# Kernel optimization log

Hardware: AMD Instinct MI355X
Metric: run time of the kernel (lower is better)

Reference implementation:

```python
import jax, jax.numpy as jnp
import numpy as np

B, H, P, D, NF = 4, 8, 196, 64, 8


def setup_inputs() -> dict:
    key = jax.random.key(0)
    ks = jax.random.split(key, 10)
    grid = (jnp.arange(NF * 5, dtype=jnp.float32) + 1.0).reshape(5, NF)
    inv = 1.0 / np.sqrt(D)
    return {
        "q": jax.random.normal(ks[0], (B, H, P, D), jnp.float32),
        "k": jax.random.normal(ks[1], (B, H, P, D), jnp.float32),
        "scale": jnp.ones((1,), jnp.float32),  # accepted but unused (as in original)
        "grid": grid,
        "grid_outer": grid,
        "base_weight": jax.random.uniform(ks[2], (D, D), jnp.float32),
        "coef_q": jax.random.uniform(ks[3], (D, NF, 5), jnp.float32),
        "coef_k": jax.random.uniform(ks[4], (D, NF, 5), jnp.float32),
        "coef_qk": jax.random.uniform(ks[5], (P * P, NF, 5), jnp.float32),
        "scale_base": jnp.ones((1, H, 5, P, D), jnp.float32),
        "scale_sp": jnp.ones((1, H, 5, P, D), jnp.float32),
        "coef_qk_outer": jnp.ones((1, 1, 5, P, P), jnp.float32),
        "lin_q_w": jax.random.uniform(ks[6], (5 * D, D), jnp.float32, -inv, inv),
        "lin_q_b": jax.random.uniform(ks[7], (5 * D,), jnp.float32, -inv, inv),
        "lin_k_w": jax.random.uniform(ks[8], (5 * D, D), jnp.float32, -inv, inv),
        "lin_k_b": jax.random.uniform(ks[9], (5 * D,), jnp.float32, -inv, inv),
    }


def reference(q, k, scale, grid, grid_outer, base_weight, coef_q, coef_k, coef_qk,
              scale_base, scale_sp, coef_qk_outer, lin_q_w, lin_q_b, lin_k_w, lin_k_b):
    b, h, p, d = q.shape
    nf = grid.shape[1]
    qf = q.reshape(-1, d)
    kf = k.reshape(-1, d)
    # lin_q / lin_k -> [B*H*P, 5, D]
    q5 = (qf @ lin_q_w.T + lin_q_b).reshape(-1, 5, d)
    k5 = (kf @ lin_k_w.T + lin_k_b).reshape(-1, 5, d)
    # base path (note: reshape [BHP,5,D] -> [B,H,5,P,D] is a raw row-major remap, as in torch)
    base_q = (jax.nn.silu(q5) @ base_weight.T).reshape(b, h, 5, p, d)
    base_k = (jax.nn.silu(k5) @ base_weight.T).reshape(b, h, 5, p, d)
    # inner sin-basis expansion: sin(grid * x) weighted by coef, summed over num_f
    cq = jnp.transpose(coef_q, (2, 1, 0))  # [5, nf, d]
    ck = jnp.transpose(coef_k, (2, 1, 0))
    sin_q = jnp.sin(grid[None, :, :, None] * q5[:, :, None, :])  # [BHP,5,nf,d]
    f_q = (sin_q * cq[None]).reshape(b, h, 5, nf, p, d).sum(3)   # [B,H,5,P,D]
    sin_k = jnp.sin(grid[None, :, :, None] * k5[:, :, None, :])
    f_k = (sin_k * ck[None]).reshape(b, h, 5, nf, p, d).sum(3)
    f_q = f_q * scale_sp + base_q * scale_base
    f_k = f_k * scale_sp + base_k * scale_base
    # sum_d(sigmoid(q)_d + sigmoid(k)_d) == sum_d sig(q) + sum_d sig(k): outer add of reductions
    aq = jax.nn.sigmoid(f_q).sum(-1)  # [B,H,5,P]
    ak = jax.nn.sigmoid(f_k).sum(-1)
    qk = (aq[..., :, None] + ak[..., None, :]).reshape(b * h, 5, p * p)
    # outer sin-basis expansion over the P*P score map
    cqk = jnp.transpose(coef_qk, (2, 1, 0))  # [5, nf, P*P]
    sin_qk = jnp.sin(grid_outer[None, :, :, None] * qk[:, :, None, :])  # [BH,5,nf,PP]
    f = (sin_qk * cqk[None]).reshape(b, h, 5, nf, p, p).sum(3)  # [B,H,5,P,P]
    f = (f * coef_qk_outer).sum(2)  # [B,H,P,P]
    return jax.nn.softmax(f, axis=-1)
```

## Files before the change

kernel.cpp:

```cpp
#include <hip/hip_runtime.h>
#include <math.h>

#define BHP 6272

__global__ __launch_bounds__(256) void k0w_pack(
    const float* __restrict__ Wq, const float* __restrict__ Wk,
    const float* __restrict__ BW, float4* __restrict__ Wq4,
    float4* __restrict__ Wk4, float4* __restrict__ BW4)
{
  const int e = blockIdx.x * 256 + threadIdx.x;
  if (e < 5120) {
    const int o = e % 320, c4 = e / 320;
    Wq4[e] = *reinterpret_cast<const float4*>(Wq + o * 64 + c4 * 4);
  } else if (e < 10240) {
    const int e2 = e - 5120;
    const int o = e2 % 320, c4 = e2 / 320;
    Wk4[e2] = *reinterpret_cast<const float4*>(Wk + o * 64 + c4 * 4);
  } else if (e < 11264) {
    const int e2 = e - 10240;
    const int d = e2 % 64, c4 = e2 / 64;
    BW4[e2] = *reinterpret_cast<const float4*>(BW + d * 64 + c4 * 4);
  }
}

__global__ __launch_bounds__(320) void k1_lin_base(
    const float* __restrict__ qx, const float* __restrict__ kx,
    const float4* __restrict__ Wq4, const float* __restrict__ bq_,
    const float4* __restrict__ Wk4, const float* __restrict__ bk_,
    const float4* __restrict__ BW4,
    float* __restrict__ y5q, float* __restrict__ y5k,
    float* __restrict__ baseq, float* __restrict__ basek)
{
  const bool kside = blockIdx.x >= (BHP / 8);
  const float* x = kside ? kx : qx;
  const float4* W4 = kside ? Wk4 : Wq4;
  const float* bias = kside ? bk_ : bq_;
  float* y5 = kside ? y5k : y5q;
  float* basef = kside ? basek : baseq;
  const int r0 = (kside ? blockIdx.x - BHP / 8 : blockIdx.x) * 8;

  __shared__ float xs[8][64];
  __shared__ float sy[8][320];
  const int t = threadIdx.x;
  for (int idx = t; idx < 8 * 64; idx += 320)
    xs[idx >> 6][idx & 63] = x[(size_t)(r0 + (idx >> 6)) * 64 + (idx & 63)];
  __syncthreads();

  const int o = t;
  float4 w[16];
  {
#pragma unroll
    for (int c4 = 0; c4 < 16; ++c4) w[c4] = W4[c4 * 320 + o];
    float acc[8];
#pragma unroll
    for (int rr = 0; rr < 8; ++rr) acc[rr] = 0.f;
#pragma unroll
    for (int c4 = 0; c4 < 16; ++c4) {
#pragma unroll
      for (int rr = 0; rr < 8; ++rr) {
        const float4 x4 = *reinterpret_cast<const float4*>(&xs[rr][c4 * 4]);
        acc[rr] = fmaf(x4.x, w[c4].x, acc[rr]);
        acc[rr] = fmaf(x4.y, w[c4].y, acc[rr]);
        acc[rr] = fmaf(x4.z, w[c4].z, acc[rr]);
        acc[rr] = fmaf(x4.w, w[c4].w, acc[rr]);
      }
    }
    const float bb = bias[o];
#pragma unroll
    for (int rr = 0; rr < 8; ++rr) {
      const float y = acc[rr] + bb;
      y5[(size_t)(r0 + rr) * 320 + o] = y;
      sy[rr][o] = y / (1.f + __expf(-y));
    }
  }
  __syncthreads();
  {
    const int s = o >> 6, d = o & 63;
#pragma unroll
    for (int c4 = 0; c4 < 16; ++c4) w[c4] = BW4[c4 * 64 + d];
    float acc[8];
#pragma unroll
    for (int rr = 0; rr < 8; ++rr) acc[rr] = 0.f;
#pragma unroll
    for (int c4 = 0; c4 < 16; ++c4) {
#pragma unroll
      for (int rr = 0; rr < 8; ++rr) {
        const float4 x4 =
            *reinterpret_cast<const float4*>(&sy[rr][s * 64 + c4 * 4]);
        acc[rr] = fmaf(x4.x, w[c4].x, acc[rr]);
        acc[rr] = fmaf(x4.y, w[c4].y, acc[rr]);
        acc[rr] = fmaf(x4.z, w[c4].z, acc[rr]);
        acc[rr] = fmaf(x4.w, w[c4].w, acc[rr]);
      }
    }
#pragma unroll
    for (int rr = 0; rr < 8; ++rr)
      basef[(size_t)(r0 + rr) * 320 + o] = acc[rr];
  }
}

__global__ __launch_bounds__(1024) void k2_act(
    const float* __restrict__ y5q, const float* __restrict__ bq,
    const float* __restrict__ y5k, const float* __restrict__ bk,
    const float* __restrict__ gridI,
    const float* __restrict__ cq, const float* __restrict__ ck,
    const float* __restrict__ ssp, const float* __restrict__ sbase,
    float* __restrict__ aq, float* __restrict__ ak)
{
  __shared__ float cl[40][65];
  __shared__ float gli[40];
  const int t = threadIdx.x;
  const int wave = t >> 6, lane = t & 63;
  const int gi = blockIdx.x * 16 + wave;
  const bool kside = gi >= 31360;
  const int idx = kside ? gi - 31360 : gi;

  {
    const float* coef = kside ? ck : cq;
    for (int e = t; e < 2560; e += 1024) {
      const int d = e / 40, r = e % 40;
      const int f = r / 5, s = r % 5;
      cl[s * 8 + f][d] = coef[e];
    }
    if (t < 40) gli[t] = gridI[t];
  }
  __syncthreads();

  const int p2 = idx % 196;
  const int s2 = (idx / 196) % 5;
  const int bh = idx / 980;
  const int h = bh & 7;
  const int d = lane;
  const int i0 = s2 * 196 + p2;
  const float* y5 = kside ? y5k : y5q;
  const float* basef = kside ? bk : bq;
  const float basev =
      basef[(size_t)(bh * 196 + i0 / 5) * 320 + (i0 % 5) * 64 + d];

  const int j0 = s2 * 1568 + p2;
  int p = j0 / 40;
  int m = j0 % 40;
  const float* y5b = y5 + (size_t)bh * 196 * 320 + d;
  float fv = 0.f;
#pragma unroll
  for (int f2 = 0; f2 < 8; ++f2) {
    const float g = gli[m];
    const float qv = y5b[p * 320 + (m >> 3) * 64];
    fv = fmaf(__sinf(g * qv), cl[m][d], fv);
    p += 4; m += 36;
    if (m >= 40) { m -= 40; p += 1; }
  }
  const int so = ((h * 5 + s2) * 196 + p2) * 64 + d;
  const float v = fv * ssp[so] + basev * sbase[so];
  float sg = 1.f / (1.f + __expf(-v));
#pragma unroll
  for (int off = 32; off > 0; off >>= 1) sg += __shfl_xor(sg, off);
  if (lane == 0) (kside ? ak : aq)[idx] = sg;
}

__global__ __launch_bounds__(256) void k2b_tab(
    const float* __restrict__ aq, const float* __restrict__ ak,
    const float* __restrict__ go, float2* __restrict__ tq,
    float2* __restrict__ tk)
{
  const int n = blockIdx.x * 256 + threadIdx.x;
  const bool kside = n >= 250880;
  const int i2 = kside ? n - 250880 : n;
  const int p = i2 % 196;
  const int m = (i2 / 196) % 40;
  const int bh = i2 / 7840;
  const float g = rintf(go[m]);
  const float a = (kside ? ak : aq)[bh * 980 + (m >> 3) * 196 + p];
  const float n0 = rintf(a * 0.15915494309f);
  float r = fmaf(n0, -6.28318548f, a);
  r = fmaf(n0, 1.74845553e-7f, r);
  const float u = g * r;
  float2* tab = kside ? tk : tq;
  tab[bh * 7840 + m * 196 + p] = make_float2(__sinf(u), __cosf(u));
}

__global__ __launch_bounds__(256) void k0_fuse(
    const float* __restrict__ cqk, const float* __restrict__ cqo,
    float* __restrict__ F)
{
  const int i = blockIdx.x;
  const int t = threadIdx.x;
  __shared__ float ld[196 * 41];
  const float4* src = reinterpret_cast<const float4*>(cqk + (size_t)i * 7840);
  for (int e4 = t; e4 < 1960; e4 += 256) {
    const float4 v = src[e4];
    const int flat = e4 * 4;
    const int j = flat / 40, m0 = flat % 40;
    float* dst = &ld[j * 41 + m0];
    dst[0] = v.x; dst[1] = v.y; dst[2] = v.z; dst[3] = v.w;
  }
  __syncthreads();
  for (int e = t; e < 7840; e += 256) {
    const int mq = e / 196, j = e % 196;
    const int s = mq >> 3, f = mq & 7;
    const float val = ld[j * 41 + f * 5 + s];
    F[(size_t)i * 7840 + e] = val * cqo[(s * 196 + i) * 196 + j];
  }
}

__global__ __launch_bounds__(256) void k3_outer(
    const float2* __restrict__ tq, const float2* __restrict__ tk,
    const float* __restrict__ F, float* __restrict__ out)
{
  const int t = threadIdx.x;
  const int wave = t >> 6, lane = t & 63;
  const int bid = blockIdx.x;
  const int swz = (bid & 7) * 98 + (bid >> 3);
  const int i = swz >> 2;
  const int bhg = swz & 3;
  const int bh0 = bhg * 8 + wave * 2;
  __shared__ float fs[7840];
  __shared__ float2 sqs[8][40];

  {
    const float4* Fp = reinterpret_cast<const float4*>(F + (size_t)i * 7840);
    float4* fs4 = reinterpret_cast<float4*>(fs);
    for (int e = t; e < 1960; e += 256) fs4[e] = Fp[e];
    for (int e = t; e < 320; e += 256) {
      const int bi = e / 40, mm = e % 40;
      sqs[bi][mm] = tq[(size_t)(bhg * 8 + bi) * 7840 + mm * 196 + i];
    }
  }
  __syncthreads();

  const bool hasb = lane < 34;
  const int ja = 2 * lane;
  const int jb = hasb ? (128 + 2 * lane) : (2 * lane);
  const float2* tk0 = tk + (size_t)bh0 * 7840;
  const float2* tk1 = tk0 + 7840;
  const int w2 = wave * 2;

  float a0x = 0.f, a0y = 0.f, a1x = 0.f, a1y = 0.f;
  float b0x = 0.f, b0y = 0.f, b1x = 0.f, b1y = 0.f;
#pragma unroll 2
  for (int mm = 0; mm < 40; ++mm) {
    const int o = mm * 196;
    const float2 fa = *reinterpret_cast<const float2*>(&fs[o + ja]);
    const float2 fb = *reinterpret_cast<const float2*>(&fs[o + jb]);
    const float2 s0 = sqs[w2][mm];
    const float2 s1 = sqs[w2 + 1][mm];
    const float4 k0a = *reinterpret_cast<const float4*>(&tk0[o + ja]);
    const float4 k0b = *reinterpret_cast<const float4*>(&tk0[o + jb]);
    const float4 k1a = *reinterpret_cast<const float4*>(&tk1[o + ja]);
    const float4 k1b = *reinterpret_cast<const float4*>(&tk1[o + jb]);
    a0x = fmaf(fmaf(s0.x, k0a.y, s0.y * k0a.x), fa.x, a0x);
    a0y = fmaf(fmaf(s0.x, k0a.w, s0.y * k0a.z), fa.y, a0y);
    a1x = fmaf(fmaf(s0.x, k0b.y, s0.y * k0b.x), fb.x, a1x);
    a1y = fmaf(fmaf(s0.x, k0b.w, s0.y * k0b.z), fb.y, a1y);
    b0x = fmaf(fmaf(s1.x, k1a.y, s1.y * k1a.x), fa.x, b0x);
    b0y = fmaf(fmaf(s1.x, k1a.w, s1.y * k1a.z), fa.y, b0y);
    b1x = fmaf(fmaf(s1.x, k1b.y, s1.y * k1b.x), fb.x, b1x);
    b1y = fmaf(fmaf(s1.x, k1b.w, s1.y * k1b.z), fb.y, b1y);
  }

  {
    const float mB = hasb ? fmaxf(a1x, a1y) : -INFINITY;
    float mx = fmaxf(fmaxf(a0x, a0y), mB);
#pragma unroll
    for (int off = 32; off > 0; off >>= 1) mx = fmaxf(mx, __shfl_xor(mx, off));
    const float e0 = __expf(a0x - mx);
    const float e1 = __expf(a0y - mx);
    const float e2 = hasb ? __expf(a1x - mx) : 0.f;
    const float e3 = hasb ? __expf(a1y - mx) : 0.f;
    float ss = e0 + e1 + e2 + e3;
#pragma unroll
    for (int off = 32; off > 0; off >>= 1) ss += __shfl_xor(ss, off);
    const float inv = 1.f / ss;
    float2* op = reinterpret_cast<float2*>(out + (size_t)(bh0 * 196 + i) * 196);
    op[lane] = make_float2(e0 * inv, e1 * inv);
    if (hasb) op[64 + lane] = make_float2(e2 * inv, e3 * inv);
  }
  {
    const float mB = hasb ? fmaxf(b1x, b1y) : -INFINITY;
    float mx = fmaxf(fmaxf(b0x, b0y), mB);
#pragma unroll
    for (int off = 32; off > 0; off >>= 1) mx = fmaxf(mx, __shfl_xor(mx, off));
    const float e0 = __expf(b0x - mx);
    const float e1 = __expf(b0y - mx);
    const float e2 = hasb ? __expf(b1x - mx) : 0.f;
    const float e3 = hasb ? __expf(b1y - mx) : 0.f;
    float ss = e0 + e1 + e2 + e3;
#pragma unroll
    for (int off = 32; off > 0; off >>= 1) ss += __shfl_xor(ss, off);
    const float inv = 1.f / ss;
    float2* op =
        reinterpret_cast<float2*>(out + (size_t)((bh0 + 1) * 196 + i) * 196);
    op[lane] = make_float2(e0 * inv, e1 * inv);
    if (hasb) op[64 + lane] = make_float2(e2 * inv, e3 * inv);
  }
}

extern "C" void kernel_launch(void* const* d_in, const int* in_sizes, int n_in,
                              void* d_out, int out_size, void* d_ws, size_t ws_size,
                              hipStream_t stream) {
  const float* q          = (const float*)d_in[0];
  const float* k          = (const float*)d_in[1];
  const float* grid       = (const float*)d_in[3];
  const float* grid_outer = (const float*)d_in[4];
  const float* base_w     = (const float*)d_in[5];
  const float* coef_q     = (const float*)d_in[6];
  const float* coef_k     = (const float*)d_in[7];
  const float* coef_qk    = (const float*)d_in[8];
  const float* scale_base = (const float*)d_in[9];
  const float* scale_sp   = (const float*)d_in[10];
  const float* cqo        = (const float*)d_in[11];
  const float* lqw        = (const float*)d_in[12];
  const float* lqb        = (const float*)d_in[13];
  const float* lkw        = (const float*)d_in[14];
  const float* lkb        = (const float*)d_in[15];
  float* out = (float*)d_out;

  const size_t SLAB = (size_t)BHP * 320;
  float* q5 = (float*)d_ws;
  float* k5 = q5 + SLAB;
  float* bq = k5 + SLAB;
  float* bk = bq + SLAB;
  float* aq = bk + SLAB;
  float* ak = aq + 32 * 5 * 196;
  float* wpack = ak + 32 * 5 * 196;
  float4* Wq4 = (float4*)wpack;
  float4* Wk4 = Wq4 + 5120;
  float4* BW4 = Wk4 + 5120;
  float* F = bq;
  float2* tabq = (float2*)bk;
  float2* tabk = tabq + 32 * 40 * 196;

  k0w_pack<<<dim3(44), dim3(256), 0, stream>>>(lqw, lkw, base_w, Wq4, Wk4, BW4);
  k1_lin_base<<<dim3(2 * BHP / 8), dim3(320), 0, stream>>>(
      q, k, Wq4, lqb, Wk4, lkb, BW4, q5, k5, bq, bk);
  k2_act<<<dim3(62720 / 16), dim3(1024), 0, stream>>>(
      q5, bq, k5, bk, grid, coef_q, coef_k, scale_sp, scale_base, aq, ak);
  k2b_tab<<<dim3(501760 / 256), dim3(256), 0, stream>>>(
      aq, ak, grid_outer, tabq, tabk);
  k0_fuse<<<dim3(196), dim3(256), 0, stream>>>(coef_qk, cqo, F);
  k3_outer<<<dim3(784), dim3(256), 0, stream>>>(tabq, tabk, F, out);
}
```

Before: 99.77 us.

## Split linear and base GEMM kernels, drop shared staging, double rows per block

The fused linear+SiLU+base-weight kernel is split into two kernels that pass the SiLU output through a new global workspace slab instead of shared memory. Each block now handles 16 rows instead of 8, and inputs are read directly from global memory as broadcast float4 loads rather than staged in LDS. The aim is to remove the intra-block barriers and LDS traffic and to amortize the weight register loads over more rows. In exchange it adds an extra launch, writes and re-reads about 16 MB of intermediate data through global memory, and halves the block count.

Result: slower. 110.4 us (+10.7%).

```diff
diff --git a/kernel.cpp b/kernel.cpp
--- a/kernel.cpp
+++ b/kernel.cpp
@@ -23,80 +23,87 @@
   }
 }
 
-__global__ __launch_bounds__(320) void k1_lin_base(
+__global__ __launch_bounds__(320) void k1_lin(
     const float* __restrict__ qx, const float* __restrict__ kx,
     const float4* __restrict__ Wq4, const float* __restrict__ bq_,
     const float4* __restrict__ Wk4, const float* __restrict__ bk_,
-    const float4* __restrict__ BW4,
     float* __restrict__ y5q, float* __restrict__ y5k,
-    float* __restrict__ baseq, float* __restrict__ basek)
-{
-  const bool kside = blockIdx.x >= (BHP / 8);
+    float* __restrict__ syq, float* __restrict__ syk)
+{
+  const bool kside = blockIdx.x >= 392;
   const float* x = kside ? kx : qx;
   const float4* W4 = kside ? Wk4 : Wq4;
   const float* bias = kside ? bk_ : bq_;
   float* y5 = kside ? y5k : y5q;
+  float* sy = kside ? syk : syq;
+  const int r0 = (kside ? blockIdx.x - 392 : blockIdx.x) * 16;
+  const int o = threadIdx.x;
+
+  float4 w[16];
+#pragma unroll
+  for (int c4 = 0; c4 < 16; ++c4) w[c4] = W4[c4 * 320 + o];
+  float acc[16];
+#pragma unroll
+  for (int rr = 0; rr < 16; ++rr) acc[rr] = 0.f;
+
+  const float* xb = x + (size_t)r0 * 64;
+#pragma unroll
+  for (int c4 = 0; c4 < 16; ++c4) {
+#pragma unroll
+    for (int rr = 0; rr < 16; ++rr) {
+      const float4 x4 =
+          *reinterpret_cast<const float4*>(xb + rr * 64 + c4 * 4);
+      acc[rr] = fmaf(x4.x, w[c4].x, acc[rr]);
+      acc[rr] = fmaf(x4.y, w[c4].y, acc[rr]);
+      acc[rr] = fmaf(x4.z, w[c4].z, acc[rr]);
+      acc[rr] = fmaf(x4.w, w[c4].w, acc[rr]);
+    }
+  }
+  const float bb = bias[o];
+#pragma unroll
+  for (int rr = 0; rr < 16; ++rr) {
+    const float y = acc[rr] + bb;
+    y5[(size_t)(r0 + rr) * 320 + o] = y;
+    sy[(size_t)(r0 + rr) * 320 + o] = y / (1.f + __expf(-y));
+  }
+}
+
+__global__ __launch_bounds__(320) void k1_base(
+    const float* __restrict__ syq, const float* __restrict__ syk,
+    const float4* __restrict__ BW4,
+    float* __restrict__ baseq, float* __restrict__ basek)
+{
+  const bool kside = blockIdx.x >= 392;
+  const float* sy = kside ? syk : syq;
   float* basef = kside ? basek : baseq;
-  const int r0 = (kside ? blockIdx.x - BHP / 8 : blockIdx.x) * 8;
-
-  __shared__ float xs[8][64];
-  __shared__ float sy[8][320];
-  const int t = threadIdx.x;
-  for (int idx = t; idx < 8 * 64; idx += 320)
-    xs[idx >> 6][idx & 63] = x[(size_t)(r0 + (idx >> 6)) * 64 + (idx & 63)];
-  __syncthreads();
-
-  const int o = t;
+  const int r0 = (kside ? blockIdx.x - 392 : blockIdx.x) * 16;
+  const int o = threadIdx.x;
+  const int s = __builtin_amdgcn_readfirstlane(o >> 6);
+  const int d = o & 63;
+
   float4 w[16];
-  {
-#pragma unroll
-    for (int c4 = 0; c4 < 16; ++c4) w[c4] = W4[c4 * 320 + o];
-    float acc[8];
-#pragma unroll
-    for (int rr = 0; rr < 8; ++rr) acc[rr] = 0.f;
-#pragma unroll
-    for (int c4 = 0; c4 < 16; ++c4) {
-#pragma unroll
-      for (int rr = 0; rr < 8; ++rr) {
-        const float4 x4 = *reinterpret_cast<const float4*>(&xs[rr][c4 * 4]);
-        acc[rr] = fmaf(x4.x, w[c4].x, acc[rr]);
-        acc[rr] = fmaf(x4.y, w[c4].y, acc[rr]);
-        acc[rr] = fmaf(x4.z, w[c4].z, acc[rr]);
-        acc[rr] = fmaf(x4.w, w[c4].w, acc[rr]);
-      }
+#pragma unroll
+  for (int c4 = 0; c4 < 16; ++c4) w[c4] = BW4[c4 * 64 + d];
+  float acc[16];
+#pragma unroll
+  for (int rr = 0; rr < 16; ++rr) acc[rr] = 0.f;
+
+  const float* syb = sy + (size_t)r0 * 320 + s * 64;
+#pragma unroll
+  for (int c4 = 0; c4 < 16; ++c4) {
+#pragma unroll
+    for (int rr = 0; rr < 16; ++rr) {
+      const float4 s4 =
+          *reinterpret_cast<const float4*>(syb + rr * 320 + c4 * 4);
+      acc[rr] = fmaf(s4.x, w[c4].x, acc[rr]);
+      acc[rr] = fmaf(s4.y, w[c4].y, acc[rr]);
+      acc[rr] = fmaf(s4.z, w[c4].z, acc[rr]);
+      acc[rr] = fmaf(s4.w, w[c4].w, acc[rr]);
     }
-    const float bb = bias[o];
-#pragma unroll
-    for (int rr = 0; rr < 8; ++rr) {
-      const float y = acc[rr] + bb;
-      y5[(size_t)(r0 + rr) * 320 + o] = y;
-      sy[rr][o] = y / (1.f + __expf(-y));
-    }
-  }
-  __syncthreads();
-  {
-    const int s = o >> 6, d = o & 63;
-#pragma unroll
-    for (int c4 = 0; c4 < 16; ++c4) w[c4] = BW4[c4 * 64 + d];
-    float acc[8];
-#pragma unroll
-    for (int rr = 0; rr < 8; ++rr) acc[rr] = 0.f;
-#pragma unroll
-    for (int c4 = 0; c4 < 16; ++c4) {
-#pragma unroll
-      for (int rr = 0; rr < 8; ++rr) {
-        const float4 x4 =
-            *reinterpret_cast<const float4*>(&sy[rr][s * 64 + c4 * 4]);
-        acc[rr] = fmaf(x4.x, w[c4].x, acc[rr]);
-        acc[rr] = fmaf(x4.y, w[c4].y, acc[rr]);
-        acc[rr] = fmaf(x4.z, w[c4].z, acc[rr]);
-        acc[rr] = fmaf(x4.w, w[c4].w, acc[rr]);
-      }
-    }
-#pragma unroll
-    for (int rr = 0; rr < 8; ++rr)
-      basef[(size_t)(r0 + rr) * 320 + o] = acc[rr];
-  }
+  }
+#pragma unroll
+  for (int rr = 0; rr < 16; ++rr)
+    basef[(size_t)(r0 + rr) * 320 + o] = acc[rr];
 }
 
 __global__ __launch_bounds__(1024) void k2_act(
@@ -320,7 +327,9 @@
   float* k5 = q5 + SLAB;
   float* bq = k5 + SLAB;
   float* bk = bq + SLAB;
-  float* aq = bk + SLAB;
+  float* syq = bk + SLAB;
+  float* syk = syq + SLAB;
+  float* aq = syk + SLAB;
   float* ak = aq + 32 * 5 * 196;
   float* wpack = ak + 32 * 5 * 196;
   float4* Wq4 = (float4*)wpack;
@@ -331,8 +340,9 @@
   float2* tabk = tabq + 32 * 40 * 196;
 
   k0w_pack<<<dim3(44), dim3(256), 0, stream>>>(lqw, lkw, base_w, Wq4, Wk4, BW4);
-  k1_lin_base<<<dim3(2 * BHP / 8), dim3(320), 0, stream>>>(
-      q, k, Wq4, lqb, Wk4, lkb, BW4, q5, k5, bq, bk);
+  k1_lin<<<dim3(784), dim3(320), 0, stream>>>(
+      q, k, Wq4, lqb, Wk4, lkb, q5, k5, syq, syk);
+  k1_base<<<dim3(784), dim3(320), 0, stream>>>(syq, syk, BW4, bq, bk);
   k2_act<<<dim3(62720 / 16), dim3(1024), 0, stream>>>(
       q5, bq, k5, bk, grid, coef_q, coef_k, scale_sp, scale_base, aq, ak);
   k2b_tab<<<dim3(501760 / 256), dim3(256), 0, stream>>>(
```
